# Optimization experiments

Measured on AMD Instinct MI355X. Metric: run time of the kernel, lower is better.

## Reference

```python
import jax, jax.numpy as jnp
import numpy as np

N_NODES = 50000
N_EDGES = 800000
N_GRAPHS = 64
IN_DIM = 768
HID = 256
OUT_DIM = 4
N_REL = 3
N_LAYERS = 3


def setup_inputs() -> dict:
    key = jax.random.key(0)
    ks = jax.random.split(key, 20)
    inp = {
        "x": jax.random.normal(ks[0], (N_NODES, IN_DIM), dtype=jnp.float32),
        "edge_index": jax.random.randint(ks[1], (2, N_EDGES), 0, N_NODES, dtype=jnp.int32),
        "edge_type": jax.random.randint(ks[2], (N_EDGES,), 0, N_REL, dtype=jnp.int32),
        "batch": jnp.sort(jax.random.randint(ks[3], (N_NODES,), 0, N_GRAPHS, dtype=jnp.int32)),
        # input projection
        "in_w": jax.random.normal(ks[4], (IN_DIM, HID), dtype=jnp.float32) * (IN_DIM ** -0.5),
        "in_b": jnp.zeros((HID,), dtype=jnp.float32),
        # RGCN layers (stacked over num_layers)
        "root_w": jax.random.normal(ks[5], (N_LAYERS, HID, HID), dtype=jnp.float32) * (HID ** -0.5),
        "rel_w": jax.random.normal(ks[6], (N_LAYERS, N_REL, HID, HID), dtype=jnp.float32) * (HID ** -0.5),
        "conv_b": jnp.zeros((N_LAYERS, HID), dtype=jnp.float32),
        "ln_w": jnp.ones((N_LAYERS, HID), dtype=jnp.float32),
        "ln_b": jnp.zeros((N_LAYERS, HID), dtype=jnp.float32),
        # classifier MLP
        "cls_w1": jax.random.normal(ks[7], (HID, HID), dtype=jnp.float32) * (HID ** -0.5),
        "cls_b1": jnp.zeros((HID,), dtype=jnp.float32),
        "cls_w2": jax.random.normal(ks[8], (HID, OUT_DIM), dtype=jnp.float32) * (HID ** -0.5),
        "cls_b2": jnp.zeros((OUT_DIM,), dtype=jnp.float32),
    }
    return inp


def _rgcn_conv(h, src, dst, edge_type, root, rel, bias):
    # PyG RGCNConv (default aggr='mean'): out = h @ root + sum_r mean_dst(h[src] | type==r) @ W_r + b
    n = h.shape[0]
    out = h @ root + bias
    for r in range(N_REL):
        m = (edge_type == r).astype(h.dtype)  # [E]
        msg = h[src] * m[:, None]             # gather + mask
        s = jax.ops.segment_sum(msg, dst, num_segments=n)   # [N, HID]
        cnt = jax.ops.segment_sum(m, dst, num_segments=n)   # [N]
        mean = s / jnp.maximum(cnt, 1.0)[:, None]
        out = out + mean @ rel[r]
    return out


def _layer_norm(h, w, b, eps=1e-5):
    mu = jnp.mean(h, axis=-1, keepdims=True)
    var = jnp.mean((h - mu) ** 2, axis=-1, keepdims=True)
    return (h - mu) * jax.lax.rsqrt(var + eps) * w + b


def reference(x, edge_index, edge_type, batch, in_w, in_b, root_w, rel_w, conv_b,
              ln_w, ln_b, cls_w1, cls_b1, cls_w2, cls_b2):
    src, dst = edge_index[0], edge_index[1]
    h = x @ in_w + in_b
    for i in range(N_LAYERS):
        h_new = _rgcn_conv(h, src, dst, edge_type, root_w[i], rel_w[i], conv_b[i])
        h = h_new + h  # residual (shapes always equal: HID->HID)
        h = jax.nn.relu(h)
        h = _layer_norm(h, ln_w[i], ln_b[i])
        # dropout is identity in eval mode
    # global max pool over each graph
    g = jax.ops.segment_max(h, batch, num_segments=N_GRAPHS)  # [B, HID]
    z = jax.nn.relu(g @ cls_w1 + cls_b1)
    return z @ cls_w2 + cls_b2
```

## Files before the change

kernel.cpp:

```cpp
#include <hip/hip_runtime.h>
#include <cstdint>
#include <cstddef>

#define NN 50000
#define NE 800000
#define NG 64
#define IND 768
#define HID 256
#define NREL 3
#define NLAY 3

typedef __attribute__((ext_vector_type(4))) float f32x4;
typedef __attribute__((ext_vector_type(8))) short s16x8;

__global__ void k_zero_int(int* __restrict__ p, int n) {
  int i = blockIdx.x * 256 + threadIdx.x;
  if (i < n) p[i] = 0;
}

__global__ void k_hist(const int* __restrict__ dst, int* __restrict__ deg) {
  int e = blockIdx.x * 256 + threadIdx.x;
  if (e < NE) atomicAdd(&deg[dst[e]], 1);
}

__global__ __launch_bounds__(1024) void k_scan(const int* __restrict__ deg,
                                               int* __restrict__ row_start,
                                               int* __restrict__ cursor) {
  __shared__ int wsum[16];
  int t = threadIdx.x;
  int lane = t & 63, wid = t >> 6;
  int running = 0;
  if (t == 0) row_start[0] = 0;
  for (int base = 0; base < NN; base += 4096) {
    int idx = base + t * 4;
    int4 d = *(const int4*)(deg + idx);
    int s = d.x + d.y + d.z + d.w;
    int sc = s;
    #pragma unroll
    for (int off = 1; off < 64; off <<= 1) {
      int o = __shfl_up(sc, off);
      if (lane >= off) sc += o;
    }
    if (lane == 63) wsum[wid] = sc;
    __syncthreads();
    if (t == 0) {
      int a = 0;
      #pragma unroll
      for (int i = 0; i < 16; ++i) { a += wsum[i]; wsum[i] = a; }
    }
    __syncthreads();
    int woff = (wid == 0) ? 0 : wsum[wid - 1];
    int excl = running + woff + (sc - s);
    int e0 = excl, e1 = e0 + d.x, e2 = e1 + d.y, e3 = e2 + d.z, e4 = e3 + d.w;
    if (idx     < NN) { cursor[idx]     = e0; row_start[idx + 1] = e1; }
    if (idx + 1 < NN) { cursor[idx + 1] = e1; row_start[idx + 2] = e2; }
    if (idx + 2 < NN) { cursor[idx + 2] = e2; row_start[idx + 3] = e3; }
    if (idx + 3 < NN) { cursor[idx + 3] = e3; row_start[idx + 4] = e4; }
    running += wsum[15];
    __syncthreads();
  }
}

__global__ void k_scatter(const int* __restrict__ src, const int* __restrict__ dst,
                          const int* __restrict__ ety, int* __restrict__ cursor,
                          unsigned* __restrict__ csr) {
  int e = blockIdx.x * 256 + threadIdx.x;
  if (e >= NE) return;
  int pos = atomicAdd(&cursor[dst[e]], 1);
  csr[pos] = (unsigned)src[e] | ((unsigned)ety[e] << 16);
}

__global__ void k_graph_bounds(const int* __restrict__ batch, int* __restrict__ gstart) {
  int i = blockIdx.x * 256 + threadIdx.x;
  if (i >= NN) return;
  int b = batch[i];
  int bp = (i == 0) ? -1 : batch[i - 1];
  for (int g = bp + 1; g <= b; ++g) gstart[g] = i;
  if (i == NN - 1) {
    for (int g = b + 1; g <= NG; ++g) gstart[g] = NN;
  }
}

__global__ __launch_bounds__(64) void k_aggregate(const float* __restrict__ h,
                                                  const int* __restrict__ row_start,
                                                  const unsigned* __restrict__ csr,
                                                  float* __restrict__ agg) {
  int n = blockIdx.x;
  int t = threadIdx.x;
  int s = row_start[n], e = row_start[n + 1];
  float4 a0 = {0, 0, 0, 0}, a1 = {0, 0, 0, 0}, a2 = {0, 0, 0, 0};
  int c0 = 0, c1 = 0, c2 = 0;
  __shared__ unsigned buf[64];
  auto accum = [&](unsigned p, float4 v) {
    int ty = (int)(p >> 16);
    if (ty == 0)      { a0.x += v.x; a0.y += v.y; a0.z += v.z; a0.w += v.w; c0++; }
    else if (ty == 1) { a1.x += v.x; a1.y += v.y; a1.z += v.z; a1.w += v.w; c1++; }
    else              { a2.x += v.x; a2.y += v.y; a2.z += v.z; a2.w += v.w; c2++; }
  };
  for (int base = s; base < e; base += 64) {
    int m = e - base; if (m > 64) m = 64;
    __syncthreads();
    if (t < m) buf[t] = csr[base + t];
    __syncthreads();
    int j = 0;
    for (; j + 4 <= m; j += 4) {
      unsigned p0 = buf[j], p1 = buf[j + 1], p2 = buf[j + 2], p3 = buf[j + 3];
      float4 v0 = *(const float4*)(h + (size_t)(p0 & 0xFFFF) * HID + t * 4);
      float4 v1 = *(const float4*)(h + (size_t)(p1 & 0xFFFF) * HID + t * 4);
      float4 v2 = *(const float4*)(h + (size_t)(p2 & 0xFFFF) * HID + t * 4);
      float4 v3 = *(const float4*)(h + (size_t)(p3 & 0xFFFF) * HID + t * 4);
      accum(p0, v0); accum(p1, v1); accum(p2, v2); accum(p3, v3);
    }
    for (; j < m; ++j) {
      unsigned p = buf[j];
      float4 v = *(const float4*)(h + (size_t)(p & 0xFFFF) * HID + t * 4);
      accum(p, v);
    }
  }
  float i0 = 1.f / (float)(c0 > 1 ? c0 : 1);
  float i1 = 1.f / (float)(c1 > 1 ? c1 : 1);
  float i2 = 1.f / (float)(c2 > 1 ? c2 : 1);
  float* o = agg + (size_t)n * (NREL * HID) + t * 4;
  float4 r0 = {a0.x * i0, a0.y * i0, a0.z * i0, a0.w * i0};
  float4 r1 = {a1.x * i1, a1.y * i1, a1.z * i1, a1.w * i1};
  float4 r2 = {a2.x * i2, a2.y * i2, a2.z * i2, a2.w * i2};
  *(float4*)(o)           = r0;
  *(float4*)(o + HID)     = r1;
  *(float4*)(o + 2 * HID) = r2;
}

__device__ __forceinline__ unsigned short bf16rne(float f) {
  union { float f; unsigned u; } x; x.f = f;
  unsigned r = (x.u + 0x7FFFu + ((x.u >> 16) & 1u)) >> 16;
  return (unsigned short)r;
}
__device__ __forceinline__ float bf2f(unsigned short h) {
  union { unsigned u; float f; } x; x.u = ((unsigned)h) << 16;
  return x.f;
}

__global__ void k_cvt(const float* __restrict__ s1, int K1e,
                      const float* __restrict__ s2, int Ktot,
                      unsigned short* __restrict__ hi, unsigned short* __restrict__ lo) {
  int t = blockIdx.x * 256 + threadIdx.x;
  if (t >= Ktot * 256) return;
  int c = t & 255, k = t >> 8;
  float v = (k < K1e) ? s1[(size_t)k * 256 + c] : s2[(size_t)(k - K1e) * 256 + c];
  unsigned short h = bf16rne(v);
  unsigned short l = bf16rne(v - bf2f(h));
  size_t o = ((size_t)(k >> 3) * 256 + c) * 8 + (k & 7);
  hi[o] = h; lo[o] = l;
}

__device__ __forceinline__ void load_lds16b(const void* g, void* l) {
  __builtin_amdgcn_global_load_lds(
      (const __attribute__((address_space(1))) unsigned*)g,
      (__attribute__((address_space(3))) unsigned*)l, 16, 0, 0);
}

template <int EPI>
__global__ __launch_bounds__(256, 1) void k_gemm_mfma(
    const float* __restrict__ A1, int lda1,
    const float* __restrict__ A2, int lda2, int K1,
    const unsigned short* __restrict__ Bhi, const unsigned short* __restrict__ Blo,
    const float* __restrict__ bias, const float* __restrict__ res,
    const float* __restrict__ lnw, const float* __restrict__ lnb,
    float* __restrict__ C, int M, int K) {
  __shared__ __align__(16) unsigned short AsH[4 * 64 * 8], AsL[4 * 64 * 8];
  __shared__ __align__(16) unsigned short BsH[4 * 256 * 8], BsL[4 * 256 * 8];
  __shared__ float lnred[64 * 4 * 2];
  int tid = (int)threadIdx.x;
  int lane = tid & 63, wv = tid >> 6;
  int n0 = (int)blockIdx.x * 64;
  int srow = tid >> 2, sg = tid & 3;
  int grow = n0 + srow; if (grow > M - 1) grow = M - 1;
  int c16 = lane & 15, kg = lane >> 4;
  int col0 = wv * 64;

  f32x4 acc[4][4] = {};
  int nkt = K / 32;

  float4 a0, a1;
  {
    const float* ap = A1 + (size_t)grow * lda1 + sg * 8;
    a0 = *(const float4*)ap;
    a1 = *(const float4*)(ap + 4);
  }

  for (int kt = 0; kt < nkt; ++kt) {
    __syncthreads();
    #pragma unroll
    for (int i = 0; i < 8; ++i) {
      int id = wv * 8 + i;
      const unsigned short* srcp = (id < 16) ? Bhi : Blo;
      unsigned short* dstp = (id < 16) ? BsH : BsL;
      int rem = id & 15, g = rem >> 2, ch = rem & 3;
      load_lds16b(srcp + (size_t)(kt * 4 + g) * 2048 + (ch * 64 + lane) * 8,
                  dstp + (g * 256 + ch * 64) * 8);
    }
    {
      float va[8] = {a0.x, a0.y, a0.z, a0.w, a1.x, a1.y, a1.z, a1.w};
      s16x8 hv, lv;
      #pragma unroll
      for (int j = 0; j < 8; ++j) {
        unsigned short h = bf16rne(va[j]);
        hv[j] = (short)h;
        lv[j] = (short)bf16rne(va[j] - bf2f(h));
      }
      int aoff = (sg * 64 + (srow ^ (sg << 2))) * 8;
      *(s16x8*)&AsH[aoff] = hv;
      *(s16x8*)&AsL[aoff] = lv;
    }
    __syncthreads();
    s16x8 ah[4], al[4];
    #pragma unroll
    for (int ri = 0; ri < 4; ++ri) {
      int ao = (kg * 64 + ((ri * 16 + c16) ^ (kg << 2))) * 8;
      ah[ri] = *(const s16x8*)&AsH[ao];
      al[ri] = *(const s16x8*)&AsL[ao];
    }
    int kn = (kt + 1) * 32;
    if (kn < K) {
      const float* Ap; int ld, kc;
      if (kn < K1) { Ap = A1; ld = lda1; kc = kn; }
      else         { Ap = A2; ld = lda2; kc = kn - K1; }
      const float* ap = Ap + (size_t)grow * ld + kc + sg * 8;
      a0 = *(const float4*)ap;
      a1 = *(const float4*)(ap + 4);
    }
    #pragma unroll
    for (int ci = 0; ci < 4; ++ci) {
      int bo = (kg * 256 + col0 + ci * 16 + c16) * 8;
      s16x8 bh = *(const s16x8*)&BsH[bo];
      s16x8 bl = *(const s16x8*)&BsL[bo];
      #pragma unroll
      for (int ri = 0; ri < 4; ++ri) {
        acc[ri][ci] = __builtin_amdgcn_mfma_f32_16x16x32_bf16(ah[ri], bh, acc[ri][ci], 0, 0, 0);
        acc[ri][ci] = __builtin_amdgcn_mfma_f32_16x16x32_bf16(ah[ri], bl, acc[ri][ci], 0, 0, 0);
        acc[ri][ci] = __builtin_amdgcn_mfma_f32_16x16x32_bf16(al[ri], bh, acc[ri][ci], 0, 0, 0);
      }
    }
  }

  float bw[4], lw[4], lb[4];
  #pragma unroll
  for (int ci = 0; ci < 4; ++ci) {
    int col = col0 + ci * 16 + c16;
    bw[ci] = bias[col];
    if (EPI == 1) { lw[ci] = lnw[col]; lb[ci] = lnb[col]; }
  }
  if (EPI == 0) {
    #pragma unroll
    for (int ri = 0; ri < 4; ++ri)
      #pragma unroll
      for (int q = 0; q < 4; ++q) {
        int row = n0 + ri * 16 + kg * 4 + q;
        if (row < M) {
          #pragma unroll
          for (int ci = 0; ci < 4; ++ci)
            C[(size_t)row * 256 + col0 + ci * 16 + c16] = acc[ri][ci][q] + bw[ci];
        }
      }
  } else {
    #pragma unroll
    for (int ri = 0; ri < 4; ++ri)
      #pragma unroll
      for (int q = 0; q < 4; ++q) {
        int rl = ri * 16 + kg * 4 + q;
        int rr = n0 + rl; int rc = rr < M ? rr : M - 1;
        float s = 0.f, s2 = 0.f;
        #pragma unroll
        for (int ci = 0; ci < 4; ++ci) {
          float r = res[(size_t)rc * 256 + col0 + ci * 16 + c16];
          float v = fmaxf(acc[ri][ci][q] + bw[ci] + r, 0.f);
          acc[ri][ci][q] = v;
          s += v; s2 += v * v;
        }
        #pragma unroll
        for (int m = 1; m < 16; m <<= 1) {
          s  += __shfl_xor(s, m);
          s2 += __shfl_xor(s2, m);
        }
        if (c16 == 0) {
          lnred[(rl * 4 + wv) * 2]     = s;
          lnred[(rl * 4 + wv) * 2 + 1] = s2;
        }
      }
    __syncthreads();
    #pragma unroll
    for (int ri = 0; ri < 4; ++ri)
      #pragma unroll
      for (int q = 0; q < 4; ++q) {
        int rl = ri * 16 + kg * 4 + q;
        float S = 0.f, S2 = 0.f;
        #pragma unroll
        for (int w = 0; w < 4; ++w) {
          S  += lnred[(rl * 4 + w) * 2];
          S2 += lnred[(rl * 4 + w) * 2 + 1];
        }
        float mean = S * (1.f / 256.f);
        float var = S2 * (1.f / 256.f) - mean * mean;
        float rstd = rsqrtf(var + 1e-5f);
        int row = n0 + rl;
        if (row < M) {
          #pragma unroll
          for (int ci = 0; ci < 4; ++ci)
            C[(size_t)row * 256 + col0 + ci * 16 + c16] =
                (acc[ri][ci][q] - mean) * rstd * lw[ci] + lb[ci];
        }
      }
  }
}

__global__ __launch_bounds__(256) void k_pool1(const float* __restrict__ h,
                                               const int* __restrict__ gstart,
                                               float* __restrict__ part) {
  int gi = blockIdx.x, ck = blockIdx.y;
  int c = (int)threadIdx.x;
  int s = gstart[gi], e = gstart[gi + 1], len = e - s;
  int cs = s + (int)(((long long)len * ck) >> 3);
  int ce = s + (int)(((long long)len * (ck + 1)) >> 3);
  float m = -3.402823466e+38f;
  int n = cs;
  for (; n + 2 <= ce; n += 2) {
    float x0 = h[(size_t)n * HID + c];
    float x1 = h[(size_t)(n + 1) * HID + c];
    m = fmaxf(m, fmaxf(x0, x1));
  }
  if (n < ce) m = fmaxf(m, h[(size_t)n * HID + c]);
  part[((size_t)gi * 8 + ck) * HID + c] = m;
}

__global__ __launch_bounds__(256) void k_pool2(const float* __restrict__ part,
                                               float* __restrict__ g) {
  int gi = blockIdx.x, c = (int)threadIdx.x;
  float m = part[((size_t)gi * 8) * HID + c];
  #pragma unroll
  for (int k = 1; k < 8; ++k) m = fmaxf(m, part[((size_t)gi * 8 + k) * HID + c]);
  g[gi * HID + c] = m;
}

__global__ __launch_bounds__(256) void k_classifier(const float* __restrict__ g,
                                                    const float* __restrict__ w1,
                                                    const float* __restrict__ b1,
                                                    const float* __restrict__ w2,
                                                    const float* __restrict__ b2,
                                                    float* __restrict__ out) {
  int gi = blockIdx.x, t = (int)threadIdx.x;
  __shared__ float gs[HID], zs[HID];
  gs[t] = g[gi * HID + t];
  __syncthreads();
  float s = b1[t];
  for (int k = 0; k < HID; ++k) s = fmaf(gs[k], w1[k * HID + t], s);
  zs[t] = fmaxf(s, 0.f);
  __syncthreads();
  if (t < 4) {
    float o = b2[t];
    for (int k = 0; k < HID; ++k) o = fmaf(zs[k], w2[k * 4 + t], o);
    out[gi * 4 + t] = o;
  }
}

extern "C" void kernel_launch(void* const* d_in, const int* in_sizes, int n_in,
                              void* d_out, int out_size, void* d_ws, size_t ws_size,
                              hipStream_t stream) {
  const float* x      = (const float*)d_in[0];
  const int*   eidx   = (const int*)d_in[1];
  const int*   etype  = (const int*)d_in[2];
  const int*   batch  = (const int*)d_in[3];
  const float* in_w   = (const float*)d_in[4];
  const float* in_b   = (const float*)d_in[5];
  const float* root_w = (const float*)d_in[6];
  const float* rel_w  = (const float*)d_in[7];
  const float* conv_b = (const float*)d_in[8];
  const float* ln_w   = (const float*)d_in[9];
  const float* ln_b   = (const float*)d_in[10];
  const float* cls_w1 = (const float*)d_in[11];
  const float* cls_b1 = (const float*)d_in[12];
  const float* cls_w2 = (const float*)d_in[13];
  const float* cls_b2 = (const float*)d_in[14];
  float* out = (float*)d_out;

  char* ws = (char*)d_ws;
  size_t off = 0;
  auto alloc = [&](size_t bytes) -> void* {
    void* p = ws + off;
    off += (bytes + 255) & ~(size_t)255;
    return p;
  };
  float*    bufA      = (float*)alloc(sizeof(float) * (size_t)NN * HID);
  float*    bufB      = (float*)alloc(sizeof(float) * (size_t)NN * HID);
  float*    agg       = (float*)alloc(sizeof(float) * (size_t)NN * NREL * HID);
  unsigned* csr       = (unsigned*)alloc(sizeof(unsigned) * NE);
  int*      deg       = (int*)alloc(sizeof(int) * 53248);
  int*      row_start = (int*)alloc(sizeof(int) * (NN + 1));
  int*      cursor    = (int*)alloc(sizeof(int) * NN);
  int*      gstart    = (int*)alloc(sizeof(int) * (NG + 1));
  float*    gpool     = (float*)alloc(sizeof(float) * NG * HID);
  float*    gpart     = (float*)alloc(sizeof(float) * NG * 8 * HID);
  unsigned short* wInH = (unsigned short*)alloc(sizeof(unsigned short) * 96 * 256 * 8);
  unsigned short* wInL = (unsigned short*)alloc(sizeof(unsigned short) * 96 * 256 * 8);
  unsigned short* wLH[NLAY];
  unsigned short* wLL[NLAY];
  for (int L = 0; L < NLAY; ++L) {
    wLH[L] = (unsigned short*)alloc(sizeof(unsigned short) * 128 * 256 * 8);
    wLL[L] = (unsigned short*)alloc(sizeof(unsigned short) * 128 * 256 * 8);
  }
  (void)ws_size; (void)in_sizes; (void)n_in; (void)out_size;

  const int* esrc = eidx;
  const int* edst = eidx + NE;

  k_cvt<<<IND, 256, 0, stream>>>(in_w, IND, nullptr, IND, wInH, wInL);
  for (int L = 0; L < NLAY; ++L)
    k_cvt<<<HID + NREL * HID, 256, 0, stream>>>(
        root_w + (size_t)L * HID * HID, HID,
        rel_w + (size_t)L * NREL * HID * HID, HID + NREL * HID, wLH[L], wLL[L]);

  k_zero_int<<<(53248 + 255) / 256, 256, 0, stream>>>(deg, 53248);
  k_hist<<<(NE + 255) / 256, 256, 0, stream>>>(edst, deg);
  k_scan<<<1, 1024, 0, stream>>>(deg, row_start, cursor);
  k_scatter<<<(NE + 255) / 256, 256, 0, stream>>>(esrc, edst, etype, cursor, csr);
  k_graph_bounds<<<(NN + 255) / 256, 256, 0, stream>>>(batch, gstart);

  int gemm_grid = (NN + 63) / 64;
  k_gemm_mfma<0><<<gemm_grid, 256, 0, stream>>>(
      x, IND, nullptr, 0, IND, wInH, wInL, in_b,
      nullptr, nullptr, nullptr, bufA, NN, IND);

  float* hcur = bufA;
  float* hnext = bufB;
  for (int L = 0; L < NLAY; ++L) {
    k_aggregate<<<NN, 64, 0, stream>>>(hcur, row_start, csr, agg);
    k_gemm_mfma<1><<<gemm_grid, 256, 0, stream>>>(
        hcur, HID, agg, NREL * HID, HID, wLH[L], wLL[L],
        conv_b + L * HID, hcur, ln_w + L * HID, ln_b + L * HID,
        hnext, NN, HID + NREL * HID);
    float* tmp = hcur; hcur = hnext; hnext = tmp;
  }

  k_pool1<<<dim3(NG, 8), 256, 0, stream>>>(hcur, gstart, gpart);
  k_pool2<<<NG, 256, 0, stream>>>(gpart, gpool);
  k_classifier<<<NG, 256, 0, stream>>>(gpool, cls_w1, cls_b1, cls_w2, cls_b2, out);
}
```

Measured before the change: 1.559 ms.

## Pre-split activations into bf16 hi/lo and double-buffer B tiles in layer GEMM

The aggregate kernel and GEMM epilogues now write the bf16 hi/lo split of their outputs directly. The layer GEMM can therefore load pre-split A fragments straight from global memory into registers instead of converting fp32 tiles and staging them through LDS. The layer GEMM also double-buffers its B tiles in LDS and prefetches the next A fragments, needing one barrier per k-step instead of two. In exchange there is extra hi/lo buffer memory and more epilogue stores, the aggregate loop loses its 4-way unroll, and A loads become strided, uncoalesced register gathers.

```diff
diff --git a/kernel.cpp b/kernel.cpp
--- a/kernel.cpp
+++ b/kernel.cpp
@@ -12,6 +12,7 @@
 
 typedef __attribute__((ext_vector_type(4))) float f32x4;
 typedef __attribute__((ext_vector_type(8))) short s16x8;
+typedef __attribute__((ext_vector_type(4))) unsigned short u16x4;
 
 __global__ void k_zero_int(int* __restrict__ p, int n) {
   int i = blockIdx.x * 256 + threadIdx.x;
@@ -81,62 +82,61 @@
   }
 }
 
+__device__ __forceinline__ unsigned short bf16rne(float f) {
+  union { float f; unsigned u; } x; x.f = f;
+  unsigned r = (x.u + 0x7FFFu + ((x.u >> 16) & 1u)) >> 16;
+  return (unsigned short)r;
+}
+__device__ __forceinline__ float bf2f(unsigned short h) {
+  union { unsigned u; float f; } x; x.u = ((unsigned)h) << 16;
+  return x.f;
+}
+
 __global__ __launch_bounds__(64) void k_aggregate(const float* __restrict__ h,
                                                   const int* __restrict__ row_start,
                                                   const unsigned* __restrict__ csr,
-                                                  float* __restrict__ agg) {
+                                                  unsigned short* __restrict__ aggH,
+                                                  unsigned short* __restrict__ aggL) {
   int n = blockIdx.x;
   int t = threadIdx.x;
   int s = row_start[n], e = row_start[n + 1];
   float4 a0 = {0, 0, 0, 0}, a1 = {0, 0, 0, 0}, a2 = {0, 0, 0, 0};
   int c0 = 0, c1 = 0, c2 = 0;
   __shared__ unsigned buf[64];
-  auto accum = [&](unsigned p, float4 v) {
-    int ty = (int)(p >> 16);
-    if (ty == 0)      { a0.x += v.x; a0.y += v.y; a0.z += v.z; a0.w += v.w; c0++; }
-    else if (ty == 1) { a1.x += v.x; a1.y += v.y; a1.z += v.z; a1.w += v.w; c1++; }
-    else              { a2.x += v.x; a2.y += v.y; a2.z += v.z; a2.w += v.w; c2++; }
-  };
   for (int base = s; base < e; base += 64) {
     int m = e - base; if (m > 64) m = 64;
     __syncthreads();
     if (t < m) buf[t] = csr[base + t];
     __syncthreads();
-    int j = 0;
-    for (; j + 4 <= m; j += 4) {
-      unsigned p0 = buf[j], p1 = buf[j + 1], p2 = buf[j + 2], p3 = buf[j + 3];
-      float4 v0 = *(const float4*)(h + (size_t)(p0 & 0xFFFF) * HID + t * 4);
-      float4 v1 = *(const float4*)(h + (size_t)(p1 & 0xFFFF) * HID + t * 4);
-      float4 v2 = *(const float4*)(h + (size_t)(p2 & 0xFFFF) * HID + t * 4);
-      float4 v3 = *(const float4*)(h + (size_t)(p3 & 0xFFFF) * HID + t * 4);
-      accum(p0, v0); accum(p1, v1); accum(p2, v2); accum(p3, v3);
-    }
-    for (; j < m; ++j) {
+    for (int j = 0; j < m; ++j) {
       unsigned p = buf[j];
-      float4 v = *(const float4*)(h + (size_t)(p & 0xFFFF) * HID + t * 4);
-      accum(p, v);
+      int src = p & 0xFFFF;
+      int ty = (int)(p >> 16);
+      float4 v = *(const float4*)(h + (size_t)src * HID + t * 4);
+      if (ty == 0)      { a0.x += v.x; a0.y += v.y; a0.z += v.z; a0.w += v.w; c0++; }
+      else if (ty == 1) { a1.x += v.x; a1.y += v.y; a1.z += v.z; a1.w += v.w; c1++; }
+      else              { a2.x += v.x; a2.y += v.y; a2.z += v.z; a2.w += v.w; c2++; }
     }
   }
   float i0 = 1.f / (float)(c0 > 1 ? c0 : 1);
   float i1 = 1.f / (float)(c1 > 1 ? c1 : 1);
   float i2 = 1.f / (float)(c2 > 1 ? c2 : 1);
-  float* o = agg + (size_t)n * (NREL * HID) + t * 4;
-  float4 r0 = {a0.x * i0, a0.y * i0, a0.z * i0, a0.w * i0};
-  float4 r1 = {a1.x * i1, a1.y * i1, a1.z * i1, a1.w * i1};
-  float4 r2 = {a2.x * i2, a2.y * i2, a2.z * i2, a2.w * i2};
-  *(float4*)(o)           = r0;
-  *(float4*)(o + HID)     = r1;
-  *(float4*)(o + 2 * HID) = r2;
-}
-
-__device__ __forceinline__ unsigned short bf16rne(float f) {
-  union { float f; unsigned u; } x; x.f = f;
-  unsigned r = (x.u + 0x7FFFu + ((x.u >> 16) & 1u)) >> 16;
-  return (unsigned short)r;
-}
-__device__ __forceinline__ float bf2f(unsigned short h) {
-  union { unsigned u; float f; } x; x.u = ((unsigned)h) << 16;
-  return x.f;
+  float vr[12] = {a0.x * i0, a0.y * i0, a0.z * i0, a0.w * i0,
+                  a1.x * i1, a1.y * i1, a1.z * i1, a1.w * i1,
+                  a2.x * i2, a2.y * i2, a2.z * i2, a2.w * i2};
+  size_t ob = (size_t)n * (NREL * HID) + t * 4;
+  #pragma unroll
+  for (int r = 0; r < 3; ++r) {
+    u16x4 hv, lv;
+    #pragma unroll
+    for (int j = 0; j < 4; ++j) {
+      unsigned short hh = bf16rne(vr[r * 4 + j]);
+      hv[j] = hh;
+      lv[j] = bf16rne(vr[r * 4 + j] - bf2f(hh));
+    }
+    *(u16x4*)(aggH + ob + r * HID) = hv;
+    *(u16x4*)(aggL + ob + r * HID) = lv;
+  }
 }
 
 __global__ void k_cvt(const float* __restrict__ s1, int K1e,
@@ -158,17 +158,15 @@
       (__attribute__((address_space(3))) unsigned*)l, 16, 0, 0);
 }
 
-template <int EPI>
-__global__ __launch_bounds__(256, 1) void k_gemm_mfma(
-    const float* __restrict__ A1, int lda1,
-    const float* __restrict__ A2, int lda2, int K1,
+__global__ __launch_bounds__(256, 1) void k_gemm_in(
+    const float* __restrict__ A1,
     const unsigned short* __restrict__ Bhi, const unsigned short* __restrict__ Blo,
-    const float* __restrict__ bias, const float* __restrict__ res,
-    const float* __restrict__ lnw, const float* __restrict__ lnb,
-    float* __restrict__ C, int M, int K) {
+    const float* __restrict__ bias,
+    float* __restrict__ C, unsigned short* __restrict__ Ch, unsigned short* __restrict__ Cl,
+    int M) {
+  const int K = IND;
   __shared__ __align__(16) unsigned short AsH[4 * 64 * 8], AsL[4 * 64 * 8];
   __shared__ __align__(16) unsigned short BsH[4 * 256 * 8], BsL[4 * 256 * 8];
-  __shared__ float lnred[64 * 4 * 2];
   int tid = (int)threadIdx.x;
   int lane = tid & 63, wv = tid >> 6;
   int n0 = (int)blockIdx.x * 64;
@@ -182,7 +180,7 @@
 
   float4 a0, a1;
   {
-    const float* ap = A1 + (size_t)grow * lda1 + sg * 8;
+    const float* ap = A1 + (size_t)grow * IND + sg * 8;
     a0 = *(const float4*)ap;
     a1 = *(const float4*)(ap + 4);
   }
@@ -221,10 +219,7 @@
     }
     int kn = (kt + 1) * 32;
     if (kn < K) {
-      const float* Ap; int ld, kc;
-      if (kn < K1) { Ap = A1; ld = lda1; kc = kn; }
-      else         { Ap = A2; ld = lda2; kc = kn - K1; }
-      const float* ap = Ap + (size_t)grow * ld + kc + sg * 8;
+      const float* ap = A1 + (size_t)grow * IND + kn + sg * 8;
       a0 = *(const float4*)ap;
       a1 = *(const float4*)(ap + 4);
     }
@@ -242,74 +237,166 @@
     }
   }
 
+  float bw[4];
+  #pragma unroll
+  for (int ci = 0; ci < 4; ++ci) bw[ci] = bias[col0 + ci * 16 + c16];
+  #pragma unroll
+  for (int ri = 0; ri < 4; ++ri)
+    #pragma unroll
+    for (int q = 0; q < 4; ++q) {
+      int row = n0 + ri * 16 + kg * 4 + q;
+      if (row < M) {
+        #pragma unroll
+        for (int ci = 0; ci < 4; ++ci) {
+          float v = acc[ri][ci][q] + bw[ci];
+          size_t o = (size_t)row * 256 + col0 + ci * 16 + c16;
+          C[o] = v;
+          unsigned short hh = bf16rne(v);
+          Ch[o] = hh;
+          Cl[o] = bf16rne(v - bf2f(hh));
+        }
+      }
+    }
+}
+
+__global__ __launch_bounds__(256, 1) void k_gemm_L(
+    const unsigned short* __restrict__ Ah1, const unsigned short* __restrict__ Al1,
+    const unsigned short* __restrict__ Ah2, const unsigned short* __restrict__ Al2,
+    const unsigned short* __restrict__ Bhi, const unsigned short* __restrict__ Blo,
+    const float* __restrict__ bias, const float* __restrict__ res,
+    const float* __restrict__ lnw, const float* __restrict__ lnb,
+    float* __restrict__ C, unsigned short* __restrict__ Ch, unsigned short* __restrict__ Cl,
+    int M) {
+  const int K1 = HID, K = HID + NREL * HID;
+  __shared__ __align__(16) unsigned short BsH[2][4 * 256 * 8];
+  __shared__ __align__(16) unsigned short BsL[2][4 * 256 * 8];
+  __shared__ float lnred[64 * 4 * 2];
+  int tid = (int)threadIdx.x;
+  int lane = tid & 63, wv = tid >> 6;
+  int n0 = (int)blockIdx.x * 64;
+  int c16 = lane & 15, kg = lane >> 4;
+  int col0 = wv * 64;
+  int arow[4];
+  #pragma unroll
+  for (int ri = 0; ri < 4; ++ri) {
+    int r = n0 + ri * 16 + c16;
+    arow[ri] = r < M ? r : M - 1;
+  }
+
+  f32x4 acc[4][4] = {};
+
+  auto dmaB = [&](int kt, int b) {
+    #pragma unroll
+    for (int i = 0; i < 8; ++i) {
+      int id = wv * 8 + i;
+      const unsigned short* srcp = (id < 16) ? Bhi : Blo;
+      unsigned short* dstp = (id < 16) ? &BsH[b][0] : &BsL[b][0];
+      int rem = id & 15, g = rem >> 2, ch = rem & 3;
+      load_lds16b(srcp + (size_t)(kt * 4 + g) * 2048 + (ch * 64 + lane) * 8,
+                  dstp + (g * 256 + ch * 64) * 8);
+    }
+  };
+  s16x8 ah[4], al[4], ahn[4] = {}, aln[4] = {};
+  auto loadA = [&](int kt, s16x8* AH, s16x8* AL) {
+    int kk = kt * 32;
+    const unsigned short *ph, *pl; int ld, kc;
+    if (kk < K1) { ph = Ah1; pl = Al1; ld = HID; kc = kk; }
+    else         { ph = Ah2; pl = Al2; ld = NREL * HID; kc = kk - K1; }
+    #pragma unroll
+    for (int ri = 0; ri < 4; ++ri) {
+      size_t o = (size_t)arow[ri] * ld + kc + kg * 8;
+      AH[ri] = *(const s16x8*)(ph + o);
+      AL[ri] = *(const s16x8*)(pl + o);
+    }
+  };
+
+  dmaB(0, 0);
+  loadA(0, ah, al);
+  int cur = 0;
+  const int nkt = K / 32;
+  for (int kt = 0; kt < nkt; ++kt) {
+    __syncthreads();
+    if (kt + 1 < nkt) {
+      dmaB(kt + 1, cur ^ 1);
+      loadA(kt + 1, ahn, aln);
+    }
+    #pragma unroll
+    for (int ci = 0; ci < 4; ++ci) {
+      int bo = (kg * 256 + col0 + ci * 16 + c16) * 8;
+      s16x8 bh = *(const s16x8*)&BsH[cur][bo];
+      s16x8 bl = *(const s16x8*)&BsL[cur][bo];
+      #pragma unroll
+      for (int ri = 0; ri < 4; ++ri) {
+        acc[ri][ci] = __builtin_amdgcn_mfma_f32_16x16x32_bf16(ah[ri], bh, acc[ri][ci], 0, 0, 0);
+        acc[ri][ci] = __builtin_amdgcn_mfma_f32_16x16x32_bf16(ah[ri], bl, acc[ri][ci], 0, 0, 0);
+        acc[ri][ci] = __builtin_amdgcn_mfma_f32_16x16x32_bf16(al[ri], bh, acc[ri][ci], 0, 0, 0);
+      }
+    }
+    #pragma unroll
+    for (int ri = 0; ri < 4; ++ri) { ah[ri] = ahn[ri]; al[ri] = aln[ri]; }
+    cur ^= 1;
+  }
+
   float bw[4], lw[4], lb[4];
   #pragma unroll
   for (int ci = 0; ci < 4; ++ci) {
     int col = col0 + ci * 16 + c16;
     bw[ci] = bias[col];
-    if (EPI == 1) { lw[ci] = lnw[col]; lb[ci] = lnb[col]; }
-  }
-  if (EPI == 0) {
-    #pragma unroll
-    for (int ri = 0; ri < 4; ++ri)
-      #pragma unroll
-      for (int q = 0; q < 4; ++q) {
-        int row = n0 + ri * 16 + kg * 4 + q;
-        if (row < M) {
-          #pragma unroll
-          for (int ci = 0; ci < 4; ++ci)
-            C[(size_t)row * 256 + col0 + ci * 16 + c16] = acc[ri][ci][q] + bw[ci];
-        }
-      }
-  } else {
-    #pragma unroll
-    for (int ri = 0; ri < 4; ++ri)
-      #pragma unroll
-      for (int q = 0; q < 4; ++q) {
-        int rl = ri * 16 + kg * 4 + q;
-        int rr = n0 + rl; int rc = rr < M ? rr : M - 1;
-        float s = 0.f, s2 = 0.f;
+    lw[ci] = lnw[col];
+    lb[ci] = lnb[col];
+  }
+  #pragma unroll
+  for (int ri = 0; ri < 4; ++ri)
+    #pragma unroll
+    for (int q = 0; q < 4; ++q) {
+      int rl = ri * 16 + kg * 4 + q;
+      int rr = n0 + rl; int rc = rr < M ? rr : M - 1;
+      float s = 0.f, s2 = 0.f;
+      #pragma unroll
+      for (int ci = 0; ci < 4; ++ci) {
+        float r = res[(size_t)rc * 256 + col0 + ci * 16 + c16];
+        float v = fmaxf(acc[ri][ci][q] + bw[ci] + r, 0.f);
+        acc[ri][ci][q] = v;
+        s += v; s2 += v * v;
+      }
+      #pragma unroll
+      for (int m = 1; m < 16; m <<= 1) {
+        s  += __shfl_xor(s, m);
+        s2 += __shfl_xor(s2, m);
+      }
+      if (c16 == 0) {
+        lnred[(rl * 4 + wv) * 2]     = s;
+        lnred[(rl * 4 + wv) * 2 + 1] = s2;
+      }
+    }
+  __syncthreads();
+  #pragma unroll
+  for (int ri = 0; ri < 4; ++ri)
+    #pragma unroll
+    for (int q = 0; q < 4; ++q) {
+      int rl = ri * 16 + kg * 4 + q;
+      float S = 0.f, S2 = 0.f;
+      #pragma unroll
+      for (int w = 0; w < 4; ++w) {
+        S  += lnred[(rl * 4 + w) * 2];
+        S2 += lnred[(rl * 4 + w) * 2 + 1];
+      }
+      float mean = S * (1.f / 256.f);
+      float var = S2 * (1.f / 256.f) - mean * mean;
+      float rstd = rsqrtf(var + 1e-5f);
+      int row = n0 + rl;
+      if (row < M) {
         #pragma unroll
         for (int ci = 0; ci < 4; ++ci) {
-          float r = res[(size_t)rc * 256 + col0 + ci * 16 + c16];
-          float v = fmaxf(acc[ri][ci][q] + bw[ci] + r, 0.f);
-          acc[ri][ci][q] = v;
-          s += v; s2 += v * v;
+          float v = (acc[ri][ci][q] - mean) * rstd * lw[ci] + lb[ci];
+          size_t o = (size_t)row * 256 + col0 + ci * 16 + c16;
+          C[o] = v;
+          unsigned short hh = bf16rne(v);
+          Ch[o] = hh;
+          Cl[o] = bf16rne(v - bf2f(hh));
         }
-        #pragma unroll
-        for (int m = 1; m < 16; m <<= 1) {
-          s  += __shfl_xor(s, m);
-          s2 += __shfl_xor(s2, m);
-        }
-        if (c16 == 0) {
-          lnred[(rl * 4 + wv) * 2]     = s;
-          lnred[(rl * 4 + wv) * 2 + 1] = s2;
-        }
-      }
-    __syncthreads();
-    #pragma unroll
-    for (int ri = 0; ri < 4; ++ri)
-      #pragma unroll
-      for (int q = 0; q < 4; ++q) {
-        int rl = ri * 16 + kg * 4 + q;
-        float S = 0.f, S2 = 0.f;
-        #pragma unroll
-        for (int w = 0; w < 4; ++w) {
-          S  += lnred[(rl * 4 + w) * 2];
-          S2 += lnred[(rl * 4 + w) * 2 + 1];
-        }
-        float mean = S * (1.f / 256.f);
-        float var = S2 * (1.f / 256.f) - mean * mean;
-        float rstd = rsqrtf(var + 1e-5f);
-        int row = n0 + rl;
-        if (row < M) {
-          #pragma unroll
-          for (int ci = 0; ci < 4; ++ci)
-            C[(size_t)row * 256 + col0 + ci * 16 + c16] =
-                (acc[ri][ci][q] - mean) * rstd * lw[ci] + lb[ci];
-        }
-      }
-  }
+      }
+    }
 }
 
 __global__ __launch_bounds__(256) void k_pool1(const float* __restrict__ h,
@@ -388,9 +475,14 @@
     off += (bytes + 255) & ~(size_t)255;
     return p;
   };
-  float*    bufA      = (float*)alloc(sizeof(float) * (size_t)NN * HID);
-  float*    bufB      = (float*)alloc(sizeof(float) * (size_t)NN * HID);
-  float*    agg       = (float*)alloc(sizeof(float) * (size_t)NN * NREL * HID);
+  float*    bufA   = (float*)alloc(sizeof(float) * (size_t)NN * HID);
+  float*    bufB   = (float*)alloc(sizeof(float) * (size_t)NN * HID);
+  unsigned short* hAh = (unsigned short*)alloc(sizeof(unsigned short) * (size_t)NN * HID);
+  unsigned short* hAl = (unsigned short*)alloc(sizeof(unsigned short) * (size_t)NN * HID);
+  unsigned short* hBh = (unsigned short*)alloc(sizeof(unsigned short) * (size_t)NN * HID);
+  unsigned short* hBl = (unsigned short*)alloc(sizeof(unsigned short) * (size_t)NN * HID);
+  unsigned short* aggH = (unsigned short*)alloc(sizeof(unsigned short) * (size_t)NN * NREL * HID);
+  unsigned short* aggL = (unsigned short*)alloc(sizeof(unsigned short) * (size_t)NN * NREL * HID);
   unsigned* csr       = (unsigned*)alloc(sizeof(unsigned) * NE);
   int*      deg       = (int*)alloc(sizeof(int) * 53248);
   int*      row_start = (int*)alloc(sizeof(int) * (NN + 1));
@@ -424,19 +516,19 @@
   k_graph_bounds<<<(NN + 255) / 256, 256, 0, stream>>>(batch, gstart);
 
   int gemm_grid = (NN + 63) / 64;
-  k_gemm_mfma<0><<<gemm_grid, 256, 0, stream>>>(
-      x, IND, nullptr, 0, IND, wInH, wInL, in_b,
-      nullptr, nullptr, nullptr, bufA, NN, IND);
-
-  float* hcur = bufA;
-  float* hnext = bufB;
+  k_gemm_in<<<gemm_grid, 256, 0, stream>>>(x, wInH, wInL, in_b, bufA, hAh, hAl, NN);
+
+  float* hcur = bufA;  unsigned short* hch = hAh;  unsigned short* hcl = hAl;
+  float* hnxt = bufB;  unsigned short* hnh = hBh;  unsigned short* hnl = hBl;
   for (int L = 0; L < NLAY; ++L) {
-    k_aggregate<<<NN, 64, 0, stream>>>(hcur, row_start, csr, agg);
-    k_gemm_mfma<1><<<gemm_grid, 256, 0, stream>>>(
-        hcur, HID, agg, NREL * HID, HID, wLH[L], wLL[L],
+    k_aggregate<<<NN, 64, 0, stream>>>(hcur, row_start, csr, aggH, aggL);
+    k_gemm_L<<<gemm_grid, 256, 0, stream>>>(
+        hch, hcl, aggH, aggL, wLH[L], wLL[L],
         conv_b + L * HID, hcur, ln_w + L * HID, ln_b + L * HID,
-        hnext, NN, HID + NREL * HID);
-    float* tmp = hcur; hcur = hnext; hnext = tmp;
+        hnxt, hnh, hnl, NN);
+    float* tf = hcur; hcur = hnxt; hnxt = tf;
+    unsigned short* th = hch; hch = hnh; hnh = th;
+    unsigned short* tl = hcl; hcl = hnl; hnl = tl;
   }
 
   k_pool1<<<dim3(NG, 8), 256, 0, stream>>>(hcur, gstart, gpart);
```

Result: faster. 1.463 ms (-6.1%).
